# Kernel optimization log

Measured on AMD Instinct MI355X. Metric: run time of the kernel, lower is better.

Reference implementation:

```python
import jax, jax.numpy as jnp
import numpy as np
from jax import lax

SAMPLES = 1024
RADIUS = 0.2
MAX_NEIGHBORS = 32


def setup_inputs() -> dict:
    key = jax.random.key(0)
    k1, k2 = jax.random.split(key)
    B, N, C = 4, 16384, 128
    xyz = jax.random.uniform(k1, (B, N, 3), dtype=jnp.float32)       # points in unit cube
    features = jax.random.normal(k2, (B, N, C), dtype=jnp.float32)
    return {"xyz": xyz, "features": features}


def farthest_point_sample(xyz, n_samples):
    """xyz: [B,N,3] -> indices [B,S] (iterative max of running min-distance)."""
    B, N, _ = xyz.shape
    first = jnp.zeros((B,), dtype=jnp.int32)

    def step(carry, _):
        min_d, last = carry                                   # [B,N], [B]
        last_pt = jnp.take_along_axis(xyz, last[:, None, None], axis=1)  # [B,1,3]
        d = jnp.sum((xyz - last_pt) ** 2, axis=-1)            # [B,N]
        min_d = jnp.minimum(min_d, d)
        nxt = jnp.argmax(min_d, axis=1).astype(jnp.int32)     # [B]
        return (min_d, nxt), nxt

    init = (jnp.full((B, N), 1e10, dtype=jnp.float32), first)
    _, rest = lax.scan(step, init, None, length=n_samples - 1)  # [S-1,B]
    return jnp.concatenate([first[None], rest], axis=0).T        # [B,S]


def ball_query(centroids, xyz, features, radius, k):
    """centroids: [B,S,3]; xyz: [B,N,3]; features: [B,N,C].
    Returns grouped xyz (centered) [B,S,K,3] and grouped features [B,S,K,C].
    Takes the first K in-radius points (by index order), padding with the
    first valid index -- matching the PointNet++ CUDA ball_query kernel."""
    B, N, _ = xyz.shape
    sqd = jnp.sum((centroids[:, :, None, :] - xyz[:, None, :, :]) ** 2, axis=-1)  # [B,S,N]
    in_ball = sqd <= radius * radius
    scores = jnp.where(in_ball, jnp.arange(N, dtype=jnp.int32), N)  # smaller = earlier valid idx
    neg_vals, idx = lax.top_k(-scores, k)                           # K smallest scores
    valid = (-neg_vals) < N                                          # [B,S,K]
    idx = jnp.where(valid, idx, idx[..., :1])                        # pad with first hit
    b = jnp.arange(B)[:, None, None]
    grouped_xyz = xyz[b, idx] - centroids[:, :, None, :]             # [B,S,K,3]
    grouped_feat = features[b, idx]                                  # [B,S,K,C]
    return grouped_xyz, grouped_feat


def reference(xyz, features):
    fps_idx = farthest_point_sample(xyz, SAMPLES)                    # [B,S]
    b = jnp.arange(xyz.shape[0])[:, None]
    centroids = lax.stop_gradient(xyz[b, fps_idx])                   # [B,S,3] (torch.no_grad)
    grouped_xyz, grouped_feat = ball_query(centroids, xyz, features, RADIUS, MAX_NEIGHBORS)
    return centroids, grouped_xyz, grouped_feat
```

## Files before the change

kernel.cpp:

```cpp
#include <hip/hip_runtime.h>
#include <cstdint>
#include <cstddef>

#define NPTS 16384
#define NSAMP 1024
#define KNBR 32
#define NCH 128


#define FPS_TPB 1024
#define NCELL 512

typedef float f32x2 __attribute__((ext_vector_type(2)));

#define PR8_FOREACH(X) X(0) X(1) X(2) X(3) X(4) X(5) X(6) X(7)

__global__ __launch_bounds__(FPS_TPB)
void fps_kernel(const float* __restrict__ xyz, float* __restrict__ centroids) {
#pragma clang fp contract(off)
  const int b = blockIdx.x;
  const int t = threadIdx.x;
  const int lane = t & 63;
  const int wave = t >> 6;
  const float* __restrict__ px = xyz + (size_t)b * NPTS * 3;

  __shared__ float A1[NPTS];
  __shared__ float A2[NPTS];
  __shared__ unsigned hist[NCELL];
  __shared__ unsigned sbase[NCELL];
  __shared__ unsigned long long s_wkey[2][16];

  float zsr[16];
  unsigned idsr[16];
  {
    float xr[16], yr[16], zr[16];
    int keys[16], dstv[16];
#pragma unroll
    for (int i = 0; i < 16; ++i) {
      const int p = i * FPS_TPB + t;
      xr[i] = px[p * 3 + 0];
      yr[i] = px[p * 3 + 1];
      zr[i] = px[p * 3 + 2];
      int cx = (int)(xr[i] * 8.0f); cx = cx < 0 ? 0 : (cx > 7 ? 7 : cx);
      int cy = (int)(yr[i] * 8.0f); cy = cy < 0 ? 0 : (cy > 7 ? 7 : cy);
      int cz = (int)(zr[i] * 8.0f); cz = cz < 0 ? 0 : (cz > 7 ? 7 : cz);
      const int mx = (cx & 1) | ((cx & 2) << 2) | ((cx & 4) << 4);
      const int my = (cy & 1) | ((cy & 2) << 2) | ((cy & 4) << 4);
      const int mz = (cz & 1) | ((cz & 2) << 2) | ((cz & 4) << 4);
      keys[i] = mx | (my << 1) | (mz << 2);
    }
    if (t < NCELL) hist[t] = 0u;
    __syncthreads();
#pragma unroll
    for (int i = 0; i < 16; ++i) atomicAdd(&hist[keys[i]], 1u);
    __syncthreads();
    if (t < NCELL) sbase[t] = hist[t];
    __syncthreads();
    for (int d = 1; d < NCELL; d <<= 1) {
      unsigned v = 0u;
      if (t < NCELL && t >= d) v = sbase[t - d];
      __syncthreads();
      if (t < NCELL) sbase[t] += v;
      __syncthreads();
    }
    if (t < NCELL) sbase[t] -= hist[t];
    __syncthreads();
    if (t < NCELL) hist[t] = 0u;
    __syncthreads();
#pragma unroll
    for (int i = 0; i < 16; ++i)
      dstv[i] = (int)(sbase[keys[i]] + atomicAdd(&hist[keys[i]], 1u));
#pragma unroll
    for (int i = 0; i < 16; ++i) {
      A1[dstv[i]] = zr[i];
      ((unsigned*)A2)[dstv[i]] = (unsigned)(i * FPS_TPB + t);
    }
    __syncthreads();
#pragma unroll
    for (int i = 0; i < 16; ++i) {
      const int u = t * 16 + i;
      zsr[i] = A1[u];
      idsr[i] = ((unsigned*)A2)[u];
    }
    __syncthreads();
#pragma unroll
    for (int i = 0; i < 16; ++i) {
      const int u = dstv[i];
      const int fi = ((u & 15) >> 1) * 2048 + (u >> 4) * 2 + (u & 1);
      A1[fi] = xr[i];
      A2[fi] = yr[i];
    }
    __syncthreads();
  }

#define DECL_PR(j) f32x2 Z##j, M##j; unsigned IDp##j;
  PR8_FOREACH(DECL_PR)
#undef DECL_PR
#define SET_PR(j)                                                     \
  Z##j = (f32x2){zsr[2 * (j)], zsr[2 * (j) + 1]};                     \
  M##j = (f32x2){1e10f, 1e10f};                                       \
  IDp##j = (idsr[2 * (j)] & 0xFFFFu) | (idsr[2 * (j) + 1] << 16);
  PR8_FOREACH(SET_PR)
#undef SET_PR

  float mnx = 1e30f, mxx = -1e30f, mny = 1e30f, mxy = -1e30f,
        mnz = 1e30f, mxz = -1e30f;
#define AABB_PR(j) {                                                  \
    const f32x2 xj = ((const f32x2*)A1)[(j) * 1024 + t];              \
    const f32x2 yj = ((const f32x2*)A2)[(j) * 1024 + t];              \
    mnx = fminf(mnx, fminf(xj.x, xj.y));                              \
    mxx = fmaxf(mxx, fmaxf(xj.x, xj.y));                              \
    mny = fminf(mny, fminf(yj.x, yj.y));                              \
    mxy = fmaxf(mxy, fmaxf(yj.x, yj.y));                              \
    mnz = fminf(mnz, fminf(Z##j.x, Z##j.y));                          \
    mxz = fmaxf(mxz, fmaxf(Z##j.x, Z##j.y)); }
  PR8_FOREACH(AABB_PR)
#undef AABB_PR
#pragma unroll
  for (int off = 1; off < 64; off <<= 1) {
    mnx = fminf(mnx, __shfl_xor(mnx, off));
    mxx = fmaxf(mxx, __shfl_xor(mxx, off));
    mny = fminf(mny, __shfl_xor(mny, off));
    mxy = fmaxf(mxy, __shfl_xor(mxy, off));
    mnz = fminf(mnz, __shfl_xor(mnz, off));
    mxz = fmaxf(mxz, __shfl_xor(mxz, off));
  }

  float lx = px[0], ly = px[1], lz = px[2];
  float svx = lx, svy = ly, svz = lz;
  unsigned long long wkc = 0ull;
  float bvw = 1e10f;

  for (int s = 1; s < NSAMP; ++s) {
    const int par = s & 1;
    const float dxb = fmaxf(fmaxf(mnx - lx, lx - mxx), 0.0f);
    const float dyb = fmaxf(fmaxf(mny - ly, ly - mxy), 0.0f);
    const float dzb = fmaxf(fmaxf(mnz - lz, lz - mxz), 0.0f);
    const float bd2 = (dxb * dxb + dyb * dyb) + dzb * dzb;
    unsigned long long wk;
    if (!(bd2 > bvw * 1.00001f)) {
      const f32x2 cx2 = {lx, lx}, cy2 = {ly, ly}, cz2 = {lz, lz};
#define UPD_PR(j) {                                                   \
      const f32x2 xj = ((const f32x2*)A1)[(j) * 1024 + t];            \
      const f32x2 yj = ((const f32x2*)A2)[(j) * 1024 + t];            \
      const f32x2 dx = xj - cx2, dy = yj - cy2, dz = Z##j - cz2;      \
      const f32x2 dd = (dx * dx + dy * dy) + dz * dz;     \
      M##j.x = fminf(M##j.x, dd.x);                                   \
      M##j.y = fminf(M##j.y, dd.y); }
      PR8_FOREACH(UPD_PR)
#undef UPD_PR
      unsigned long long nk = 0ull;
#define KEY_PR(j) {                                                   \
      const unsigned long long k1 =                                   \
          ((unsigned long long)__float_as_uint(M##j.x) << 32) |       \
          (unsigned)~(IDp##j & 0xFFFFu);                              \
      const unsigned long long k2 =                                   \
          ((unsigned long long)__float_as_uint(M##j.y) << 32) |       \
          (unsigned)~(IDp##j >> 16);                                  \
      if (k1 > nk) nk = k1;                                           \
      if (k2 > nk) nk = k2; }
      PR8_FOREACH(KEY_PR)
#undef KEY_PR
#pragma unroll
      for (int off = 1; off < 64; off <<= 1) {
        const unsigned long long ok = __shfl_xor(nk, off);
        if (ok > nk) nk = ok;
      }
      wk = nk;
      wkc = nk;
      bvw = __uint_as_float((unsigned)(nk >> 32));
    } else {
      wk = wkc;
    }
    if (lane == 0) s_wkey[par][wave] = wk;
    __syncthreads();
    unsigned long long best = s_wkey[par][lane & 15];
#pragma unroll
    for (int off = 1; off < 16; off <<= 1) {
      const unsigned long long ok = __shfl_xor(best, off);
      if (ok > best) best = ok;
    }
    const unsigned widx = (unsigned)__builtin_amdgcn_readfirstlane(
        (int)(~(unsigned)best));
    lx = px[widx * 3 + 0];
    ly = px[widx * 3 + 1];
    lz = px[widx * 3 + 2];
    if (s == t) { svx = lx; svy = ly; svz = lz; }
  }

  float* co = centroids + (size_t)b * NSAMP * 3;
  co[t * 3 + 0] = svx;
  co[t * 3 + 1] = svy;
  co[t * 3 + 2] = svz;
}

__global__ __launch_bounds__(256) void group_kernel(
    const float* __restrict__ xyz, const float* __restrict__ feat,
    const float* __restrict__ centroids,
    float* __restrict__ gxyz, float* __restrict__ gfeat) {
#pragma clang fp contract(off)
  const int gw = blockIdx.x;
  const int b = gw >> 10;
  const int tid = threadIdx.x;
  const int wave = tid >> 6;
  const int lane = tid & 63;

  const float* px = xyz + (size_t)b * NPTS * 3;
  const float* pc = centroids + (size_t)gw * 3;
  const float cx = pc[0], cy = pc[1], cz = pc[2];
  const float rr = 0.04f;

  __shared__ int sh_idx[KNBR];
  __shared__ float sh_gx[KNBR * 3];
  __shared__ unsigned long long sh_mask[2][4];

  int cnt = 0;
  for (int n0 = 0; n0 < NPTS && cnt < KNBR; n0 += 256) {
    const int ci = (n0 >> 8) & 1;
    const int p = n0 + tid;
    const float xx = px[p * 3 + 0];
    const float yy = px[p * 3 + 1];
    const float zz = px[p * 3 + 2];
    const float dx = xx - cx;
    const float dy = yy - cy;
    const float dz = zz - cz;
    const float d = (dx * dx + dy * dy) + dz * dz;
    const bool in = d <= rr;
    const unsigned long long mask = __ballot(in);
    if (lane == 0) sh_mask[ci][wave] = mask;
    __syncthreads();
    const unsigned long long m0 = sh_mask[ci][0];
    const unsigned long long m1 = sh_mask[ci][1];
    const unsigned long long m2 = sh_mask[ci][2];
    const unsigned long long m3 = sh_mask[ci][3];
    int base = cnt;
    if (wave > 0) base += (int)__popcll(m0);
    if (wave > 1) base += (int)__popcll(m1);
    if (wave > 2) base += (int)__popcll(m2);
    const int pos = base + (int)__popcll(mask & ((1ull << lane) - 1ull));
    if (in && pos < KNBR) {
      sh_idx[pos] = p;
      sh_gx[pos * 3 + 0] = dx;
      sh_gx[pos * 3 + 1] = dy;
      sh_gx[pos * 3 + 2] = dz;
    }
    cnt += (int)(__popcll(m0) + __popcll(m1) + __popcll(m2) + __popcll(m3));
  }
  if (cnt == 0 && tid == 0) {
    sh_idx[0] = 0;
    sh_gx[0] = px[0] - cx;
    sh_gx[1] = px[1] - cy;
    sh_gx[2] = px[2] - cz;
  }
  __syncthreads();

  const int nf0 = (cnt < 1) ? 1 : cnt;
  const int nf = (nf0 < KNBR) ? nf0 : KNBR;
  if (tid < KNBR && tid >= nf) {
    sh_idx[tid] = sh_idx[0];
    sh_gx[tid * 3 + 0] = sh_gx[0];
    sh_gx[tid * 3 + 1] = sh_gx[1];
    sh_gx[tid * 3 + 2] = sh_gx[2];
  }
  __syncthreads();

  float* ox = gxyz + (size_t)gw * KNBR * 3;
  if (tid < KNBR * 3) ox[tid] = sh_gx[tid];

  float* og = gfeat + (size_t)gw * KNBR * NCH;
  const float* pf = feat + (size_t)b * NPTS * NCH;
#pragma unroll
  for (int k = wave; k < KNBR; k += 4) {
    const int row = sh_idx[k];
    const float2 v = ((const float2*)(pf + (size_t)row * NCH))[lane];
    ((float2*)(og + (size_t)k * NCH))[lane] = v;
  }
}

extern "C" void kernel_launch(void* const* d_in, const int* in_sizes, int n_in,
                              void* d_out, int out_size, void* d_ws, size_t ws_size,
                              hipStream_t stream) {
  const float* xyz = (const float*)d_in[0];
  const float* feat = (const float*)d_in[1];
  float* out = (float*)d_out;
  const int B = in_sizes[0] / (NPTS * 3);

  float* centroids = out;
  float* gxyz = centroids + (size_t)B * NSAMP * 3;
  float* gfeat = gxyz + (size_t)B * NSAMP * KNBR * 3;

  fps_kernel<<<B, FPS_TPB, 0, stream>>>(xyz, centroids);
  group_kernel<<<B * NSAMP, 256, 0, stream>>>(xyz, feat, centroids, gxyz,
                                              gfeat);
}
```

Baseline: 1.544 ms.

## Broadcast winner coordinates via LDS and encode wave/slot in FPS argmax keys

The per-iteration argmax key now packs the inverted point index, the wave id and the register slot into its low bits. The owning lane publishes the winner's coordinates into a small shared array, so every thread reads the next centroid from LDS instead of doing a dependent global load of xyz after the block reduction. The distance update is rewritten with packed-FP32 inline asm, and the per-thread key max becomes a tree reduction. This shortens the serial critical path of each FPS step, at the cost of extra selection logic in the owning lane and reliance on exact key equality to pick the owner.

Result: slower. 1.780 ms (+15.2%).

```diff
diff --git a/kernel.cpp b/kernel.cpp
--- a/kernel.cpp
+++ b/kernel.cpp
@@ -29,6 +29,7 @@
   __shared__ unsigned hist[NCELL];
   __shared__ unsigned sbase[NCELL];
   __shared__ unsigned long long s_wkey[2][16];
+  __shared__ float4 s_wxyz[2][16];
 
   float zsr[16];
   unsigned idsr[16];
@@ -93,13 +94,16 @@
     __syncthreads();
   }
 
-#define DECL_PR(j) f32x2 Z##j, M##j; unsigned IDp##j;
+#define DECL_PR(j) f32x2 Z##j, M##j; unsigned LOa##j, LOb##j;
   PR8_FOREACH(DECL_PR)
 #undef DECL_PR
-#define SET_PR(j)                                                     \
-  Z##j = (f32x2){zsr[2 * (j)], zsr[2 * (j) + 1]};                     \
-  M##j = (f32x2){1e10f, 1e10f};                                       \
-  IDp##j = (idsr[2 * (j)] & 0xFFFFu) | (idsr[2 * (j) + 1] << 16);
+#define SET_PR(j)                                                         \
+  Z##j = (f32x2){zsr[2 * (j)], zsr[2 * (j) + 1]};                         \
+  M##j = (f32x2){1e10f, 1e10f};                                           \
+  LOa##j = ((idsr[2 * (j)] ^ 0x3FFFu) << 18) | ((unsigned)wave << 14) |   \
+           (unsigned)(2 * (j));                                           \
+  LOb##j = ((idsr[2 * (j) + 1] ^ 0x3FFFu) << 18) | ((unsigned)wave << 14) | \
+           (unsigned)(2 * (j) + 1);
   PR8_FOREACH(SET_PR)
 #undef SET_PR
 
@@ -128,7 +132,9 @@
 
   float lx = px[0], ly = px[1], lz = px[2];
   float svx = lx, svy = ly, svz = lz;
-  unsigned long long wkc = 0ull;
+  bool ow = false;
+  unsigned long long mykc = 0ull;
+  float wxr = 0.f, wyr = 0.f, wzr = 0.f;
   float bvw = 1e10f;
 
   for (int s = 1; s < NSAMP; ++s) {
@@ -137,54 +143,85 @@
     const float dyb = fmaxf(fmaxf(mny - ly, ly - mxy), 0.0f);
     const float dzb = fmaxf(fmaxf(mnz - lz, lz - mxz), 0.0f);
     const float bd2 = (dxb * dxb + dyb * dyb) + dzb * dzb;
-    unsigned long long wk;
     if (!(bd2 > bvw * 1.00001f)) {
       const f32x2 cx2 = {lx, lx}, cy2 = {ly, ly}, cz2 = {lz, lz};
-#define UPD_PR(j) {                                                   \
-      const f32x2 xj = ((const f32x2*)A1)[(j) * 1024 + t];            \
-      const f32x2 yj = ((const f32x2*)A2)[(j) * 1024 + t];            \
-      const f32x2 dx = xj - cx2, dy = yj - cy2, dz = Z##j - cz2;      \
-      const f32x2 dd = (dx * dx + dy * dy) + dz * dz;     \
-      M##j.x = fminf(M##j.x, dd.x);                                   \
-      M##j.y = fminf(M##j.y, dd.y); }
+#define UPD_PR(j) {                                                       \
+      const f32x2 xj = ((const f32x2*)A1)[(j) * 1024 + t];                \
+      const f32x2 yj = ((const f32x2*)A2)[(j) * 1024 + t];                \
+      f32x2 dx, dy, dz, sx, sy, sz, s1, s2;                               \
+      asm("v_pk_add_f32 %0, %1, %2 neg_lo:[0,1] neg_hi:[0,1]"             \
+          : "=v"(dx) : "v"(xj), "v"(cx2));                                \
+      asm("v_pk_add_f32 %0, %1, %2 neg_lo:[0,1] neg_hi:[0,1]"             \
+          : "=v"(dy) : "v"(yj), "v"(cy2));                                \
+      asm("v_pk_add_f32 %0, %1, %2 neg_lo:[0,1] neg_hi:[0,1]"             \
+          : "=v"(dz) : "v"(Z##j), "v"(cz2));                              \
+      asm("v_pk_mul_f32 %0, %1, %1" : "=v"(sx) : "v"(dx));                \
+      asm("v_pk_mul_f32 %0, %1, %1" : "=v"(sy) : "v"(dy));                \
+      asm("v_pk_mul_f32 %0, %1, %1" : "=v"(sz) : "v"(dz));                \
+      asm("v_pk_add_f32 %0, %1, %2" : "=v"(s1) : "v"(sx), "v"(sy));       \
+      asm("v_pk_add_f32 %0, %1, %2" : "=v"(s2) : "v"(s1), "v"(sz));       \
+      M##j.x = fminf(M##j.x, s2.x);                                       \
+      M##j.y = fminf(M##j.y, s2.y); }
       PR8_FOREACH(UPD_PR)
 #undef UPD_PR
-      unsigned long long nk = 0ull;
-#define KEY_PR(j) {                                                   \
-      const unsigned long long k1 =                                   \
-          ((unsigned long long)__float_as_uint(M##j.x) << 32) |       \
-          (unsigned)~(IDp##j & 0xFFFFu);                              \
-      const unsigned long long k2 =                                   \
-          ((unsigned long long)__float_as_uint(M##j.y) << 32) |       \
-          (unsigned)~(IDp##j >> 16);                                  \
-      if (k1 > nk) nk = k1;                                           \
-      if (k2 > nk) nk = k2; }
-      PR8_FOREACH(KEY_PR)
-#undef KEY_PR
+#define KEYS_PR(j)                                                        \
+      const unsigned long long kA##j =                                    \
+          ((unsigned long long)__float_as_uint(M##j.x) << 32) | LOa##j;   \
+      const unsigned long long kB##j =                                    \
+          ((unsigned long long)__float_as_uint(M##j.y) << 32) | LOb##j;   \
+      const unsigned long long kp##j = kA##j > kB##j ? kA##j : kB##j;
+      PR8_FOREACH(KEYS_PR)
+#undef KEYS_PR
+      const unsigned long long u0 = kp0 > kp1 ? kp0 : kp1;
+      const unsigned long long u1 = kp2 > kp3 ? kp2 : kp3;
+      const unsigned long long u2 = kp4 > kp5 ? kp4 : kp5;
+      const unsigned long long u3 = kp6 > kp7 ? kp6 : kp7;
+      const unsigned long long v0 = u0 > u1 ? u0 : u1;
+      const unsigned long long v1 = u2 > u3 ? u2 : u3;
+      const unsigned long long myk = v0 > v1 ? v0 : v1;
+      unsigned long long nk = myk;
 #pragma unroll
       for (int off = 1; off < 64; off <<= 1) {
         const unsigned long long ok = __shfl_xor(nk, off);
         if (ok > nk) nk = ok;
       }
-      wk = nk;
-      wkc = nk;
+      ow = (myk == nk);
+      if (ow) {
+        mykc = nk;
+        const int sl = (int)(nk & 15ull);
+        const int jj = sl >> 1;
+        const f32x2 xv = ((const f32x2*)A1)[jj * 1024 + t];
+        const f32x2 yv = ((const f32x2*)A2)[jj * 1024 + t];
+        f32x2 zz = Z0;
+        if (jj == 1) zz = Z1;
+        if (jj == 2) zz = Z2;
+        if (jj == 3) zz = Z3;
+        if (jj == 4) zz = Z4;
+        if (jj == 5) zz = Z5;
+        if (jj == 6) zz = Z6;
+        if (jj == 7) zz = Z7;
+        wxr = (sl & 1) ? xv.y : xv.x;
+        wyr = (sl & 1) ? yv.y : yv.x;
+        wzr = (sl & 1) ? zz.y : zz.x;
+      }
       bvw = __uint_as_float((unsigned)(nk >> 32));
-    } else {
-      wk = wkc;
-    }
-    if (lane == 0) s_wkey[par][wave] = wk;
-    __syncthreads();
-    unsigned long long best = s_wkey[par][lane & 15];
+    }
+    if (ow) {
+      s_wkey[par][wave] = mykc;
+      s_wxyz[par][wave] = make_float4(wxr, wyr, wzr, 0.0f);
+    }
+    __syncthreads();
+    unsigned long long bk = s_wkey[par][lane & 15];
 #pragma unroll
     for (int off = 1; off < 16; off <<= 1) {
-      const unsigned long long ok = __shfl_xor(best, off);
-      if (ok > best) best = ok;
-    }
-    const unsigned widx = (unsigned)__builtin_amdgcn_readfirstlane(
-        (int)(~(unsigned)best));
-    lx = px[widx * 3 + 0];
-    ly = px[widx * 3 + 1];
-    lz = px[widx * 3 + 2];
+      const unsigned long long ok = __shfl_xor(bk, off);
+      if (ok > bk) bk = ok;
+    }
+    const int wwave = (int)((bk >> 14) & 15ull);
+    const float4 wc = s_wxyz[par][wwave];
+    lx = wc.x;
+    ly = wc.y;
+    lz = wc.z;
     if (s == t) { svx = lx; svy = ly; svz = lz; }
   }
 
```
